# Performance work log

Measured on AMD Instinct MI355X. Metric: run time of the kernel, lower is better.

## Reference

```python
import jax, jax.numpy as jnp
import numpy as np
import math

HIDDEN = 1024
HEADS = 16
HEAD_DIM = HIDDEN // HEADS


def setup_inputs() -> dict:
    key = jax.random.key(0)
    ks = jax.random.split(key, 9)
    s = 1.0 / math.sqrt(HIDDEN)
    return {
        "x": jax.random.normal(ks[0], (4, 2048, HIDDEN), dtype=jnp.float32),
        "Wq": jax.random.normal(ks[1], (HIDDEN, HIDDEN), dtype=jnp.float32) * s,
        "bq": jnp.zeros((HIDDEN,), dtype=jnp.float32),
        "Wk": jax.random.normal(ks[2], (HIDDEN, HIDDEN), dtype=jnp.float32) * s,
        "bk": jnp.zeros((HIDDEN,), dtype=jnp.float32),
        "Wv": jax.random.normal(ks[3], (HIDDEN, HIDDEN), dtype=jnp.float32) * s,
        "bv": jnp.zeros((HIDDEN,), dtype=jnp.float32),
        "Wo": jax.random.normal(ks[4], (HIDDEN, HIDDEN), dtype=jnp.float32) * s,
        "bo": jnp.zeros((HIDDEN,), dtype=jnp.float32),
    }


def reference(x, Wq, bq, Wk, bk, Wv, bv, Wo, bo):
    B, L, D = x.shape
    H, hd = HEADS, HEAD_DIM
    # QKV projections (weights stored as [in, out], i.e. torch W.T)
    q = (x @ Wq + bq).reshape(B, L, H, hd).transpose(0, 2, 1, 3)  # [B,H,L,hd]
    k = (x @ Wk + bk).reshape(B, L, H, hd).transpose(0, 2, 1, 3)
    v = (x @ Wv + bv).reshape(B, L, H, hd).transpose(0, 2, 1, 3)
    scores = jnp.einsum("bhqd,bhkd->bhqk", q, k) / math.sqrt(hd)  # [B,H,L,L]
    causal_mask = jnp.triu(jnp.full((L, L), -jnp.inf, dtype=scores.dtype), k=1)
    att = jax.nn.softmax(scores + causal_mask, axis=-1)
    out = jnp.einsum("bhqk,bhkd->bhqd", att, v)  # [B,H,L,hd]
    out = out.transpose(0, 2, 1, 3).reshape(B, L, D)
    return out @ Wo + bo
```

## Files before the change

### kernel.cpp

```cpp
#include <hip/hip_runtime.h>
#include <stdint.h>

#define LOG2E 1.44269504088896340736f

typedef __attribute__((ext_vector_type(8))) short short8;
typedef __attribute__((ext_vector_type(4))) float float4v;

typedef const __attribute__((address_space(1))) unsigned int gu32;
typedef __attribute__((address_space(3))) unsigned int lu32;

__device__ __forceinline__ void async16(const unsigned short* g, unsigned short* l){
  __builtin_amdgcn_global_load_lds((gu32*)g, (lu32*)l, 16, 0, 0);
}

__device__ __forceinline__ unsigned short f2bf(float f){
  union { float f; unsigned int u; } v; v.f = f;
  unsigned int u = v.u;
  return (unsigned short)((u + 0x7FFFu + ((u >> 16) & 1u)) >> 16);
}
__device__ __forceinline__ unsigned int pkbf(float a, float b){
  union { float f; unsigned int u; } ua, ub; ua.f=a; ub.f=b;
  return ((ua.u + 0x8000u) >> 16) | ((ub.u + 0x8000u) & 0xFFFF0000u);
}

__global__ void convert_x_kernel(const float* __restrict__ x, unsigned short* __restrict__ xb){
  int t = blockIdx.x * 256 + threadIdx.x;
  const float4v* xp = (const float4v*)x;
  float4v a = xp[2*t], b = xp[2*t+1];
  short8 o;
  o[0]=(short)f2bf(a[0]); o[1]=(short)f2bf(a[1]); o[2]=(short)f2bf(a[2]); o[3]=(short)f2bf(a[3]);
  o[4]=(short)f2bf(b[0]); o[5]=(short)f2bf(b[1]); o[6]=(short)f2bf(b[2]); o[7]=(short)f2bf(b[3]);
  ((short8*)xb)[t] = o;
}

__global__ void transpose_w_kernel(const float* __restrict__ Wq, const float* __restrict__ Wk,
                                   const float* __restrict__ Wv, const float* __restrict__ Wo,
                                   unsigned short* __restrict__ wqkvT, unsigned short* __restrict__ woT){
  __shared__ float tileS[64][68];
  int mat = blockIdx.x >> 8, tile = blockIdx.x & 255;
  int tk = tile >> 4, tn = tile & 15;
  const float* W = (mat==0)?Wq:(mat==1)?Wk:(mat==2)?Wv:Wo;
  int k0 = tk*64, n0 = tn*64;
  int tid = threadIdx.x;
  #pragma unroll
  for (int it=0; it<4; ++it){
    int idx = tid + it*256;
    int r = idx >> 4, c4 = idx & 15;
    float4v v = *(const float4v*)&W[(uint64_t)(k0+r)*1024 + n0 + c4*4];
    tileS[r][c4*4+0]=v[0]; tileS[r][c4*4+1]=v[1]; tileS[r][c4*4+2]=v[2]; tileS[r][c4*4+3]=v[3];
  }
  __syncthreads();
  unsigned short* dst; int nbase;
  if (mat<3){ dst = wqkvT; nbase = mat*1024 + n0; } else { dst = woT; nbase = n0; }
  #pragma unroll
  for (int it=0; it<2; ++it){
    int idx = tid + it*256;
    int n = idx >> 3, g = idx & 7;
    short8 o;
    #pragma unroll
    for (int j=0;j<8;++j) o[j] = (short)f2bf(tileS[g*8+j][n]);
    *(short8*)&dst[(uint64_t)(nbase+n)*1024 + k0 + g*8] = o;
  }
}

template<int EPI>
__global__ __launch_bounds__(256, 2) void gemm_kernel(
    const unsigned short* __restrict__ A, const unsigned short* __restrict__ BT,
    const float* __restrict__ bias0, const float* __restrict__ bias1, const float* __restrict__ bias2,
    unsigned short* __restrict__ oq, unsigned short* __restrict__ ok,
    unsigned short* __restrict__ ov, float* __restrict__ of)
{
  __shared__ __attribute__((aligned(16))) unsigned short lS[2*128*64];
  unsigned short* lA = lS;
  unsigned short* lB = lS + 128*64;
  const int tid = threadIdx.x, lane = tid & 63, wave = tid >> 6;
  const int wr = wave >> 1, wc = wave & 1;
  const int by = blockIdx.x & 63, bx = blockIdx.x >> 6;
  const int m0 = by * 128, n0 = bx * 128;
  const int c = lane & 15, quad = lane >> 4;
  const float QSCALE = 0.125f * LOG2E;

  float4v acc[4][4];
  #pragma unroll
  for (int i=0;i<4;++i)
    #pragma unroll
    for (int j=0;j<4;++j) acc[i][j] = (float4v){0.f,0.f,0.f,0.f};

  for (int kt = 0; kt < 16; ++kt){
    __syncthreads();
    #pragma unroll
    for (int it=0; it<4; ++it){
      int gl = (wave*4+it)*64 + lane;
      int row = gl >> 3, gp = gl & 7, gs = gp ^ (row & 7);
      async16(&A[(uint64_t)(m0+row)*1024 + kt*64 + gs*8], &lA[gl*8]);
    }
    #pragma unroll
    for (int it=0; it<4; ++it){
      int gl = (wave*4+it)*64 + lane;
      int row = gl >> 3, gp = gl & 7, gs = gp ^ (row & 7);
      async16(&BT[(uint64_t)(n0+row)*1024 + kt*64 + gs*8], &lB[gl*8]);
    }
    __syncthreads();
    #pragma unroll
    for (int kk=0; kk<2; ++kk){
      short8 af[4], bf[4];
      #pragma unroll
      for (int i=0;i<4;++i){
        int row = wr*64 + i*16 + c;
        int g = (quad + kk*4) ^ (row & 7);
        af[i] = *(const short8*)&lA[row*64 + g*8];
      }
      #pragma unroll
      for (int j=0;j<4;++j){
        int row = wc*64 + j*16 + c;
        int g = (quad + kk*4) ^ (row & 7);
        bf[j] = *(const short8*)&lB[row*64 + g*8];
      }
      #pragma unroll
      for (int i=0;i<4;++i)
        #pragma unroll
        for (int j=0;j<4;++j)
          acc[i][j] = __builtin_amdgcn_mfma_f32_16x16x32_bf16(af[i], bf[j], acc[i][j], 0, 0, 0);
    }
  }

  if (EPI == 0){
    const int sel = bx >> 3;
    const int n0l = n0 & 1023;
    const int h0 = n0l >> 6;
    const int bb = m0 >> 11, l0 = m0 & 2047;
    const float* bp = (sel==0)?bias0:(sel==1)?bias1:bias2;
    float bj[4];
    #pragma unroll
    for (int j=0;j<4;++j) bj[j] = bp[n0l + wc*64 + j*16 + c];
    __syncthreads();
    if (sel < 2){
      unsigned short* dst = (sel==0)?oq:ok;
      #pragma unroll
      for (int i=0;i<4;++i){
        #pragma unroll
        for (int r=0;r<4;++r){
          int mloc = wr*64 + i*16 + quad*4 + r;
          #pragma unroll
          for (int j=0;j<4;++j){
            float v = acc[i][j][r] + bj[j];
            if (sel == 0) v *= QSCALE;
            int col = wc*64 + j*16 + c;
            int gg = col >> 3;
            int gs2 = (gg & 8) | ((gg & 7) ^ (mloc & 7));
            lS[mloc*128 + gs2*8 + (col & 7)] = f2bf(v);
          }
        }
      }
      __syncthreads();
      #pragma unroll
      for (int it=0; it<8; ++it){
        int gl = it*256 + tid;
        int row = gl >> 4, gg = gl & 15;
        int gs2 = (gg & 8) | ((gg & 7) ^ (row & 7));
        short8 w = *(const short8*)&lS[row*128 + gs2*8];
        int hh = h0 + (gg >> 3);
        *(short8*)&dst[((uint64_t)(bb*16 + hh)*2048 + l0 + row)*64 + (gg & 7)*8] = w;
      }
    } else {
      #pragma unroll
      for (int i=0;i<4;++i){
        #pragma unroll
        for (int r=0;r<4;++r){
          int mloc = wr*64 + i*16 + quad*4 + r;
          int mgg = mloc >> 3;
          #pragma unroll
          for (int j=0;j<4;++j){
            float v = acc[i][j][r] + bj[j];
            int col = wc*64 + j*16 + c;
            int gsT = (mgg & 8) | ((mgg & 7) ^ (col & 7));
            lS[col*128 + gsT*8 + (mloc & 7)] = f2bf(v);
          }
        }
      }
      __syncthreads();
      #pragma unroll
      for (int it=0; it<8; ++it){
        int idx = it*256 + tid;
        int mg = idx & 15, cc = idx >> 4;
        int gsT2 = (mg & 8) | ((mg & 7) ^ (cc & 7));
        short8 w = *(const short8*)&lS[cc*128 + gsT2*8];
        int hh = h0 + (cc >> 6), d = cc & 63;
        *(short8*)&ov[((uint64_t)(bb*16 + hh)*64 + d)*2048 + l0 + mg*8] = w;
      }
    }
  } else {
    float* lf = (float*)lS;
    float bj[4];
    #pragma unroll
    for (int j=0;j<4;++j) bj[j] = bias0[n0 + wc*64 + j*16 + c];
    #pragma unroll
    for (int half=0; half<2; ++half){
      __syncthreads();
      if (wr == half){
        #pragma unroll
        for (int i=0;i<4;++i){
          #pragma unroll
          for (int r=0;r<4;++r){
            int lrow = i*16 + quad*4 + r;
            #pragma unroll
            for (int j=0;j<4;++j){
              int col = wc*64 + j*16 + c;
              int gg = col >> 2;
              int gs2 = (gg & 24) | ((gg & 7) ^ (lrow & 7));
              lf[lrow*128 + gs2*4 + (col & 3)] = acc[i][j][r] + bj[j];
            }
          }
        }
      }
      __syncthreads();
      #pragma unroll
      for (int it=0; it<8; ++it){
        int gl = it*256 + tid;
        int lrow = gl >> 5, gg = gl & 31;
        int gs2 = (gg & 24) | ((gg & 7) ^ (lrow & 7));
        float4v w = *(const float4v*)&lf[lrow*128 + gs2*4];
        *(float4v*)&of[(uint64_t)(m0 + half*64 + lrow)*1024 + n0 + gg*4] = w;
      }
    }
  }
}

__global__ __launch_bounds__(256, 2) void attn_kernel(
    const unsigned short* __restrict__ q, const unsigned short* __restrict__ k,
    const unsigned short* __restrict__ vt, unsigned short* __restrict__ o)
{
  __shared__ __attribute__((aligned(16))) unsigned short lQ[128*64];
  __shared__ __attribute__((aligned(16))) unsigned short lK[2][64*64];
  __shared__ __attribute__((aligned(16))) unsigned short lV[2][64*64];
  __shared__ __attribute__((aligned(16))) unsigned short lP[4][32*64];

  const int idx = blockIdx.x;
  const int bh = idx & 63;
  const int qt = 15 - (idx >> 6);
  const int tid = threadIdx.x, lane = tid & 63, wave = tid >> 6;
  const int c = lane & 15, quad = lane >> 4;

  const unsigned short* qh = q  + (uint64_t)bh * (2048*64);
  const unsigned short* kh = k  + (uint64_t)bh * (2048*64);
  const unsigned short* vh = vt + (uint64_t)bh * (64*2048);

  #pragma unroll
  for (int it=0; it<4; ++it){
    int gl = (wave*4+it)*64 + lane;
    int row = gl >> 3, gp = gl & 7, gs = gp ^ (row & 7);
    async16(&qh[(uint64_t)(qt*128 + row)*64 + gs*8], &lQ[gl*8]);
  }
  #pragma unroll
  for (int it=0; it<2; ++it){
    int gl = (wave*2+it)*64 + lane;
    int row = gl >> 3, gp = gl & 7, gs = gp ^ (row & 7);
    async16(&kh[(uint64_t)row*64 + gs*8], &lK[0][gl*8]);
    async16(&vh[(uint64_t)row*2048 + gs*8], &lV[0][gl*8]);
  }

  float4v accO[2][4];
  #pragma unroll
  for (int u=0;u<2;++u)
    #pragma unroll
    for (int t=0;t<4;++t) accO[u][t] = (float4v){0.f,0.f,0.f,0.f};
  float lsum[2] = {0.f, 0.f};
  short8 qf[2][2];

  const int ktEnd = 2*qt + 1;
  unsigned short* Pw = &lP[wave][0];

  for (int kt = 0; kt <= ktEnd; ++kt){
    __syncthreads();
    const int cb = kt & 1;

    if (kt == 0){
      #pragma unroll
      for (int u=0; u<2; ++u)
        #pragma unroll
        for (int kk=0; kk<2; ++kk){
          int row = u*64 + wave*16 + c;
          int g = (kk*4 + quad) ^ (row & 7);
          qf[u][kk] = *(const short8*)&lQ[row*64 + g*8];
        }
    }
    if (kt < ktEnd){
      const int nb = 1 - cb;
      #pragma unroll
      for (int it=0; it<2; ++it){
        int gl = (wave*2+it)*64 + lane;
        int row = gl >> 3, gp = gl & 7, gs = gp ^ (row & 7);
        async16(&kh[(uint64_t)((kt+1)*64 + row)*64 + gs*8], &lK[nb][gl*8]);
        async16(&vh[(uint64_t)row*2048 + (kt+1)*64 + gs*8], &lV[nb][gl*8]);
      }
    }

    const bool doU0 = (kt != ktEnd);

    float4v s[2][4];
    #pragma unroll
    for (int u=0;u<2;++u)
      #pragma unroll
      for (int j=0;j<4;++j) s[u][j] = (float4v){0.f,0.f,0.f,0.f};
    #pragma unroll
    for (int kk=0; kk<2; ++kk){
      short8 kf[4];
      #pragma unroll
      for (int j=0;j<4;++j){
        int row = j*16 + c;
        int g = (kk*4 + quad) ^ (row & 7);
        kf[j] = *(const short8*)&lK[cb][row*64 + g*8];
      }
      #pragma unroll
      for (int j=0;j<4;++j)
        s[1][j] = __builtin_amdgcn_mfma_f32_16x16x32_bf16(kf[j], qf[1][kk], s[1][j], 0, 0, 0);
      if (doU0){
        #pragma unroll
        for (int j=0;j<4;++j)
          s[0][j] = __builtin_amdgcn_mfma_f32_16x16x32_bf16(kf[j], qf[0][kk], s[0][j], 0, 0, 0);
      }
    }

    #pragma unroll
    for (int u=0;u<2;++u){
      if (u==0 && !doU0) continue;
      const int qb_u = qt*128 + u*64 + wave*16;
      const bool needMask = (kt*64 + 63 > qb_u);
      const int qg = qb_u + c;
      #pragma unroll
      for (int j=0;j<4;++j){
        float p0,p1,p2,p3;
        {
          float4v sv = s[u][j];
          p0 = __builtin_amdgcn_exp2f(sv[0]);
          p1 = __builtin_amdgcn_exp2f(sv[1]);
          p2 = __builtin_amdgcn_exp2f(sv[2]);
          p3 = __builtin_amdgcn_exp2f(sv[3]);
        }
        if (needMask){
          int keyb = kt*64 + j*16 + quad*4;
          if (keyb + 0 > qg) p0 = 0.f;
          if (keyb + 1 > qg) p1 = 0.f;
          if (keyb + 2 > qg) p2 = 0.f;
          if (keyb + 3 > qg) p3 = 0.f;
        }
        lsum[u] += (p0 + p1) + (p2 + p3);
        int row = u*16 + c;
        int g = (2*j + (quad>>1)) ^ (row & 7);
        uint2 w; w.x = pkbf(p0,p1); w.y = pkbf(p2,p3);
        *(uint2*)&Pw[row*64 + g*8 + (quad&1)*4] = w;
      }
    }

    #pragma unroll
    for (int kk=0; kk<2; ++kk){
      short8 bv[4];
      #pragma unroll
      for (int t=0;t<4;++t){
        int row = t*16 + c;
        int g = (kk*4 + quad) ^ (row & 7);
        bv[t] = *(const short8*)&lV[cb][row*64 + g*8];
      }
      {
        int row = 16 + c;
        int g = (kk*4 + quad) ^ (row & 7);
        short8 ap = *(const short8*)&Pw[row*64 + g*8];
        #pragma unroll
        for (int t=0;t<4;++t)
          accO[1][t] = __builtin_amdgcn_mfma_f32_16x16x32_bf16(ap, bv[t], accO[1][t], 0, 0, 0);
      }
      if (doU0){
        int row = c;
        int g = (kk*4 + quad) ^ (row & 7);
        short8 ap = *(const short8*)&Pw[row*64 + g*8];
        #pragma unroll
        for (int t=0;t<4;++t)
          accO[0][t] = __builtin_amdgcn_mfma_f32_16x16x32_bf16(ap, bv[t], accO[0][t], 0, 0, 0);
      }
    }
  }

  #pragma unroll
  for (int u=0;u<2;++u){
    lsum[u] += __shfl_xor(lsum[u], 16, 64);
    lsum[u] += __shfl_xor(lsum[u], 32, 64);
  }

  const int b = bh >> 4, h = bh & 15;
  unsigned short* lPf = &lP[0][0];
  #pragma unroll
  for (int u=0;u<2;++u){
    #pragma unroll
    for (int r=0;r<4;++r){
      float ls = __shfl(lsum[u], quad*4 + r, 64);
      float rinv = 1.0f / ls;
      int mloc = u*64 + wave*16 + quad*4 + r;
      #pragma unroll
      for (int t=0;t<4;++t){
        int col = t*16 + c;
        int gg = col >> 3;
        int gs2 = gg ^ (mloc & 7);
        lPf[mloc*64 + gs2*8 + (col & 7)] = f2bf(accO[u][t][r] * rinv);
      }
    }
  }
  __syncthreads();
  #pragma unroll
  for (int it=0; it<4; ++it){
    int gl = it*256 + tid;
    int row = gl >> 3, gg = gl & 7;
    int gs2 = gg ^ (row & 7);
    short8 w = *(const short8*)&lPf[row*64 + gs2*8];
    uint64_t m = (uint64_t)b*2048 + qt*128 + row;
    *(short8*)&o[m*1024 + h*64 + gg*8] = w;
  }
}

extern "C" void kernel_launch(void* const* d_in, const int* in_sizes, int n_in,
                              void* d_out, int out_size, void* d_ws, size_t ws_size,
                              hipStream_t stream)
{
  (void)in_sizes; (void)n_in; (void)out_size; (void)ws_size;
  const float* x  = (const float*)d_in[0];
  const float* Wq = (const float*)d_in[1];
  const float* bq = (const float*)d_in[2];
  const float* Wk = (const float*)d_in[3];
  const float* bk = (const float*)d_in[4];
  const float* Wv = (const float*)d_in[5];
  const float* bv = (const float*)d_in[6];
  const float* Wo = (const float*)d_in[7];
  const float* bo = (const float*)d_in[8];
  float* out = (float*)d_out;

  char* ws = (char*)d_ws;
  unsigned short* xb    = (unsigned short*)(ws);
  unsigned short* wqkvT = (unsigned short*)(ws + (16ull<<20));
  unsigned short* woT   = (unsigned short*)(ws + (22ull<<20));
  unsigned short* qb    = (unsigned short*)(ws + (24ull<<20));
  unsigned short* kb    = (unsigned short*)(ws + (40ull<<20));
  unsigned short* vtb   = (unsigned short*)(ws + (56ull<<20));
  unsigned short* ab    = xb;

  convert_x_kernel<<<4096, 256, 0, stream>>>(x, xb);
  transpose_w_kernel<<<1024, 256, 0, stream>>>(Wq, Wk, Wv, Wo, wqkvT, woT);
  gemm_kernel<0><<<1536, 256, 0, stream>>>(xb, wqkvT, bq, bk, bv, qb, kb, vtb, nullptr);
  attn_kernel<<<1024, 256, 0, stream>>>(qb, kb, vtb, ab);
  gemm_kernel<1><<<512, 256, 0, stream>>>(ab, woT, bo, nullptr, nullptr, nullptr, nullptr, nullptr, out);
}
```

Measured before the change: 247.4 us.

## Enlarge attention query tile to 256 rows and reuse Q LDS for P

Each attention block now handles 256 query rows (four 64-row groups per wave) instead of 128, halving the grid to 512 blocks and halving K/V tile reloads per query. Q fragments are loaded into registers once up front, and the Q shared buffer is then reused for the per-wave P scratch and the output staging, removing the separate lP array. The block schedule is changed to pair long and short causal tiles. It raises register pressure (16 accumulators plus 8 Q fragments) and lowers parallelism, which risks occupancy and load imbalance.

Measured after the change: 255.0 us. 1.03x slower.

```diff
diff --git a/kernel.cpp b/kernel.cpp
--- a/kernel.cpp
+++ b/kernel.cpp
@@ -230,14 +230,14 @@
     const unsigned short* __restrict__ q, const unsigned short* __restrict__ k,
     const unsigned short* __restrict__ vt, unsigned short* __restrict__ o)
 {
-  __shared__ __attribute__((aligned(16))) unsigned short lQ[128*64];
+  __shared__ __attribute__((aligned(16))) unsigned short lQ[256*64];
   __shared__ __attribute__((aligned(16))) unsigned short lK[2][64*64];
   __shared__ __attribute__((aligned(16))) unsigned short lV[2][64*64];
-  __shared__ __attribute__((aligned(16))) unsigned short lP[4][32*64];
 
   const int idx = blockIdx.x;
   const int bh = idx & 63;
-  const int qt = 15 - (idx >> 6);
+  const int g8 = idx >> 6;
+  const int qt = (g8 < 4) ? (7 - g8) : (g8 - 4);
   const int tid = threadIdx.x, lane = tid & 63, wave = tid >> 6;
   const int c = lane & 15, quad = lane >> 4;
 
@@ -246,10 +246,10 @@
   const unsigned short* vh = vt + (uint64_t)bh * (64*2048);
 
   #pragma unroll
-  for (int it=0; it<4; ++it){
-    int gl = (wave*4+it)*64 + lane;
+  for (int it=0; it<8; ++it){
+    int gl = (wave*8+it)*64 + lane;
     int row = gl >> 3, gp = gl & 7, gs = gp ^ (row & 7);
-    async16(&qh[(uint64_t)(qt*128 + row)*64 + gs*8], &lQ[gl*8]);
+    async16(&qh[(uint64_t)(qt*256 + row)*64 + gs*8], &lQ[gl*8]);
   }
   #pragma unroll
   for (int it=0; it<2; ++it){
@@ -258,32 +258,33 @@
     async16(&kh[(uint64_t)row*64 + gs*8], &lK[0][gl*8]);
     async16(&vh[(uint64_t)row*2048 + gs*8], &lV[0][gl*8]);
   }
-
-  float4v accO[2][4];
-  #pragma unroll
-  for (int u=0;u<2;++u)
+  __syncthreads();
+
+  short8 qf[4][2];
+  #pragma unroll
+  for (int u=0; u<4; ++u)
+    #pragma unroll
+    for (int kk=0; kk<2; ++kk){
+      int row = u*64 + wave*16 + c;
+      int gq = (kk*4 + quad) ^ (row & 7);
+      qf[u][kk] = *(const short8*)&lQ[row*64 + gq*8];
+    }
+  __syncthreads();
+
+  float4v accO[4][4];
+  #pragma unroll
+  for (int u=0;u<4;++u)
     #pragma unroll
     for (int t=0;t<4;++t) accO[u][t] = (float4v){0.f,0.f,0.f,0.f};
-  float lsum[2] = {0.f, 0.f};
-  short8 qf[2][2];
-
-  const int ktEnd = 2*qt + 1;
-  unsigned short* Pw = &lP[wave][0];
+  float lsum[4] = {0.f, 0.f, 0.f, 0.f};
+
+  const int ktEnd = 4*qt + 3;
+  unsigned short* Pw = &lQ[wave*64*64];
 
   for (int kt = 0; kt <= ktEnd; ++kt){
     __syncthreads();
     const int cb = kt & 1;
 
-    if (kt == 0){
-      #pragma unroll
-      for (int u=0; u<2; ++u)
-        #pragma unroll
-        for (int kk=0; kk<2; ++kk){
-          int row = u*64 + wave*16 + c;
-          int g = (kk*4 + quad) ^ (row & 7);
-          qf[u][kk] = *(const short8*)&lQ[row*64 + g*8];
-        }
-    }
     if (kt < ktEnd){
       const int nb = 1 - cb;
       #pragma unroll
@@ -295,48 +296,41 @@
       }
     }
 
-    const bool doU0 = (kt != ktEnd);
-
-    float4v s[2][4];
-    #pragma unroll
-    for (int u=0;u<2;++u)
-      #pragma unroll
-      for (int j=0;j<4;++j) s[u][j] = (float4v){0.f,0.f,0.f,0.f};
-    #pragma unroll
-    for (int kk=0; kk<2; ++kk){
-      short8 kf[4];
+    bool act[4];
+    #pragma unroll
+    for (int u=0;u<4;++u) act[u] = (kt*64 <= qt*256 + u*64 + wave*16 + 15);
+
+    short8 kfA[2][4];
+    #pragma unroll
+    for (int kk=0; kk<2; ++kk)
       #pragma unroll
       for (int j=0;j<4;++j){
         int row = j*16 + c;
-        int g = (kk*4 + quad) ^ (row & 7);
-        kf[j] = *(const short8*)&lK[cb][row*64 + g*8];
-      }
-      #pragma unroll
-      for (int j=0;j<4;++j)
-        s[1][j] = __builtin_amdgcn_mfma_f32_16x16x32_bf16(kf[j], qf[1][kk], s[1][j], 0, 0, 0);
-      if (doU0){
+        int gk = (kk*4 + quad) ^ (row & 7);
+        kfA[kk][j] = *(const short8*)&lK[cb][row*64 + gk*8];
+      }
+
+    #pragma unroll
+    for (int u=0;u<4;++u){
+      if (u<3 && !act[u]) continue;
+      float4v s[4];
+      #pragma unroll
+      for (int j=0;j<4;++j) s[j] = (float4v){0.f,0.f,0.f,0.f};
+      #pragma unroll
+      for (int kk=0; kk<2; ++kk)
         #pragma unroll
         for (int j=0;j<4;++j)
-          s[0][j] = __builtin_amdgcn_mfma_f32_16x16x32_bf16(kf[j], qf[0][kk], s[0][j], 0, 0, 0);
-      }
-    }
-
-    #pragma unroll
-    for (int u=0;u<2;++u){
-      if (u==0 && !doU0) continue;
-      const int qb_u = qt*128 + u*64 + wave*16;
+          s[j] = __builtin_amdgcn_mfma_f32_16x16x32_bf16(kfA[kk][j], qf[u][kk], s[j], 0, 0, 0);
+
+      const int qb_u = qt*256 + u*64 + wave*16;
       const bool needMask = (kt*64 + 63 > qb_u);
       const int qg = qb_u + c;
       #pragma unroll
       for (int j=0;j<4;++j){
-        float p0,p1,p2,p3;
-        {
-          float4v sv = s[u][j];
-          p0 = __builtin_amdgcn_exp2f(sv[0]);
-          p1 = __builtin_amdgcn_exp2f(sv[1]);
-          p2 = __builtin_amdgcn_exp2f(sv[2]);
-          p3 = __builtin_amdgcn_exp2f(sv[3]);
-        }
+        float p0 = __builtin_amdgcn_exp2f(s[j][0]);
+        float p1 = __builtin_amdgcn_exp2f(s[j][1]);
+        float p2 = __builtin_amdgcn_exp2f(s[j][2]);
+        float p3 = __builtin_amdgcn_exp2f(s[j][3]);
         if (needMask){
           int keyb = kt*64 + j*16 + quad*4;
           if (keyb + 0 > qg) p0 = 0.f;
@@ -346,50 +340,46 @@
         }
         lsum[u] += (p0 + p1) + (p2 + p3);
         int row = u*16 + c;
-        int g = (2*j + (quad>>1)) ^ (row & 7);
+        int gsw = (2*j + (quad>>1)) ^ (row & 7);
         uint2 w; w.x = pkbf(p0,p1); w.y = pkbf(p2,p3);
-        *(uint2*)&Pw[row*64 + g*8 + (quad&1)*4] = w;
-      }
-    }
-
-    #pragma unroll
-    for (int kk=0; kk<2; ++kk){
-      short8 bv[4];
+        *(uint2*)&Pw[row*64 + gsw*8 + (quad&1)*4] = w;
+      }
+    }
+
+    short8 bvA[2][4];
+    #pragma unroll
+    for (int kk=0; kk<2; ++kk)
       #pragma unroll
       for (int t=0;t<4;++t){
         int row = t*16 + c;
-        int g = (kk*4 + quad) ^ (row & 7);
-        bv[t] = *(const short8*)&lV[cb][row*64 + g*8];
-      }
-      {
-        int row = 16 + c;
-        int g = (kk*4 + quad) ^ (row & 7);
-        short8 ap = *(const short8*)&Pw[row*64 + g*8];
+        int gv = (kk*4 + quad) ^ (row & 7);
+        bvA[kk][t] = *(const short8*)&lV[cb][row*64 + gv*8];
+      }
+    #pragma unroll
+    for (int u=0;u<4;++u){
+      if (u<3 && !act[u]) continue;
+      #pragma unroll
+      for (int kk=0; kk<2; ++kk){
+        int row = u*16 + c;
+        int gp2 = (kk*4 + quad) ^ (row & 7);
+        short8 ap = *(const short8*)&Pw[row*64 + gp2*8];
         #pragma unroll
         for (int t=0;t<4;++t)
-          accO[1][t] = __builtin_amdgcn_mfma_f32_16x16x32_bf16(ap, bv[t], accO[1][t], 0, 0, 0);
-      }
-      if (doU0){
-        int row = c;
-        int g = (kk*4 + quad) ^ (row & 7);
-        short8 ap = *(const short8*)&Pw[row*64 + g*8];
-        #pragma unroll
-        for (int t=0;t<4;++t)
-          accO[0][t] = __builtin_amdgcn_mfma_f32_16x16x32_bf16(ap, bv[t], accO[0][t], 0, 0, 0);
-      }
-    }
-  }
-
-  #pragma unroll
-  for (int u=0;u<2;++u){
+          accO[u][t] = __builtin_amdgcn_mfma_f32_16x16x32_bf16(ap, bvA[kk][t], accO[u][t], 0, 0, 0);
+      }
+    }
+  }
+
+  #pragma unroll
+  for (int u=0;u<4;++u){
     lsum[u] += __shfl_xor(lsum[u], 16, 64);
     lsum[u] += __shfl_xor(lsum[u], 32, 64);
   }
 
+  __syncthreads();
   const int b = bh >> 4, h = bh & 15;
-  unsigned short* lPf = &lP[0][0];
-  #pragma unroll
-  for (int u=0;u<2;++u){
+  #pragma unroll
+  for (int u=0;u<4;++u){
     #pragma unroll
     for (int r=0;r<4;++r){
       float ls = __shfl(lsum[u], quad*4 + r, 64);
@@ -400,18 +390,18 @@
         int col = t*16 + c;
         int gg = col >> 3;
         int gs2 = gg ^ (mloc & 7);
-        lPf[mloc*64 + gs2*8 + (col & 7)] = f2bf(accO[u][t][r] * rinv);
+        lQ[mloc*64 + gs2*8 + (col & 7)] = f2bf(accO[u][t][r] * rinv);
       }
     }
   }
   __syncthreads();
   #pragma unroll
-  for (int it=0; it<4; ++it){
+  for (int it=0; it<8; ++it){
     int gl = it*256 + tid;
     int row = gl >> 3, gg = gl & 7;
     int gs2 = gg ^ (row & 7);
-    short8 w = *(const short8*)&lPf[row*64 + gs2*8];
-    uint64_t m = (uint64_t)b*2048 + qt*128 + row;
+    short8 w = *(const short8*)&lQ[row*64 + gs2*8];
+    uint64_t m = (uint64_t)b*2048 + qt*256 + row;
     *(short8*)&o[m*1024 + h*64 + gg*8] = w;
   }
 }
@@ -444,6 +434,6 @@
   convert_x_kernel<<<4096, 256, 0, stream>>>(x, xb);
   transpose_w_kernel<<<1024, 256, 0, stream>>>(Wq, Wk, Wv, Wo, wqkvT, woT);
   gemm_kernel<0><<<1536, 256, 0, stream>>>(xb, wqkvT, bq, bk, bv, qb, kb, vtb, nullptr);
-  attn_kernel<<<1024, 256, 0, stream>>>(qb, kb, vtb, ab);
+  attn_kernel<<<512, 256, 0, stream>>>(qb, kb, vtb, ab);
   gemm_kernel<1><<<512, 256, 0, stream>>>(ab, woT, bo, nullptr, nullptr, nullptr, nullptr, nullptr, out);
 }
```
